# Optimization experiments

Hardware: AMD Instinct MI355X
Metric: run time of the kernel (lower is better)

The kernel has to match this reference:

```python
import jax, jax.numpy as jnp
import numpy as np

NUM_TIMESCALES = 16
MAX_TIME = 100.0
N_HEADS = 4
MLP_WIDTH = 128
HIDDEN_EACH = 128  # hidden_size // attn_n_heads = 512 // 4


def setup_inputs() -> dict:
    key = jax.random.key(0)
    ks = jax.random.split(key, 8)
    B, ROWS_PER_PAT, V = 32, 64, 32
    R = B * ROWS_PER_PAT
    # patient i has counts[i] observations, laid out row-major in its block of rows
    counts = 512 + 16 * np.arange(B)
    M = np.zeros((R, V), np.int32)
    for i in range(B):
        flat = M[i * ROWS_PER_PAT:(i + 1) * ROWS_PER_PAT].reshape(-1)
        flat[:counts[i]] = 1
    n_obs = int(counts.sum())        # 24320
    max_n_obs = int(counts.max())    # 1008
    n_in = 2 * NUM_TIMESCALES + 2    # 34

    def lin(k, o, i_):
        kw, kb = jax.random.split(k)
        return (jax.random.normal(kw, (o, i_)) * (1.0 / np.sqrt(i_)),
                jax.random.normal(kb, (o,)) * 0.01)

    W0, b0 = lin(ks[0], MLP_WIDTH, n_in)
    W1, b1 = lin(ks[1], MLP_WIDTH, MLP_WIDTH)
    W2, b2 = lin(ks[2], HIDDEN_EACH, MLP_WIDTH)
    Wq, bq = lin(ks[3], HIDDEN_EACH, HIDDEN_EACH)
    Wk, bk = lin(ks[4], HIDDEN_EACH, HIDDEN_EACH)
    return {
        "times": jax.random.uniform(ks[5], (R,)) * MAX_TIME,
        "time_ptr": jnp.arange(R + 1),
        "X": jax.random.normal(ks[6], (R, V)),
        "M": jnp.asarray(M),
        "obs_idx": jnp.repeat(jnp.arange(B), ROWS_PER_PAT),
        "pat_idx": jnp.arange(B),
        "W0": W0, "b0": b0, "W1": W1, "b1": b1, "W2": W2, "b2": b2,
        "Wq": Wq, "bq": bq, "Wk": Wk, "bk": bk,
        "n_obs": n_obs, "max_n_obs": max_n_obs,
    }


def reference(times, time_ptr, X, M, obs_idx, pat_idx,
              W0, b0, W1, b1, W2, b2, Wq, bq, Wk, bk, n_obs, max_n_obs):
    B = pat_idx.shape[0]
    # --- ragged scatter: (time_row, var) observations -> padded per-patient sets ---
    rows, cols = jnp.nonzero(M, size=n_obs)          # row-major, grouped by patient
    p = obs_idx[rows]                                # patient id per observation
    vals = X[rows, cols]
    t_arr = jnp.repeat(times, jnp.diff(time_ptr), total_repeat_length=X.shape[0])
    t = t_arr[rows]
    lens = jnp.bincount(p, length=B)
    starts = jnp.cumsum(lens) - lens
    pos = jnp.arange(n_obs) - starts[p]              # within-patient slot index
    Sv = jnp.zeros((B, max_n_obs), X.dtype).at[p, pos].set(cols.astype(X.dtype))
    Sx = jnp.zeros((B, max_n_obs), X.dtype).at[p, pos].set(vals)
    St = jnp.zeros((B, max_n_obs), X.dtype).at[p, pos].set(t)
    pad = jnp.arange(max_n_obs)[None, :] >= lens[:, None]   # True = padding
    # --- time embedding + feature concat: [sin, cos, var, value] ---
    timescales = MAX_TIME ** jnp.linspace(0.0, 1.0, NUM_TIMESCALES)
    st = St[..., None] / timescales
    new_X = jnp.concatenate([jnp.sin(st), jnp.cos(st), Sv[..., None], Sx[..., None]], axis=-1)
    # --- encoder MLP (depth 3 -> 1 hidden layer, eval mode: dropout is identity) ---
    h = jax.nn.relu(new_X @ W0.T + b0)
    h = jax.nn.relu(h @ W1.T + b1)
    enc = h @ W2.T + b2                              # [B, L, 128]
    # --- masked self-attention weights (only q/k matter; output is discarded) ---
    L = max_n_obs
    hd = HIDDEN_EACH // N_HEADS
    q = (enc @ Wq.T + bq).reshape(B, L, N_HEADS, hd)
    k = (enc @ Wk.T + bk).reshape(B, L, N_HEADS, hd)
    scores = jnp.einsum('blhd,bmhd->bhlm', q, k) / np.sqrt(hd)
    scores = jnp.where(pad[:, None, None, :], -1e30, scores)
    attn = jax.nn.softmax(scores, axis=-1)           # [B, H, L, L]
    w = attn[:, :, -1, :]                            # last-query attention row
    summed = jnp.einsum('bhl,ble->bhe', w, enc)      # [B, H, 128]
    return summed.reshape(B, -1)                     # [B, 512]
```

## Files before the change

### kernel.cpp

```cpp
#include <hip/hip_runtime.h>

#define B_PAT 32
#define RTOT 2048
#define NV 32
#define LMAX 1008
#define NTS 16
#define NIN 64
#define TLD 72
#define HW 128
#define LDSP 136
#define NCH 16
#define CH 63
#define ELD 132
#define RLD 136

typedef __attribute__((ext_vector_type(8))) short short8;
typedef __attribute__((ext_vector_type(4))) float floatx4;

__device__ __forceinline__ ushort f2b(float f) {
  unsigned int x = __float_as_uint(f);
  unsigned int r = (x + 0x7FFFu + ((x >> 16) & 1u)) >> 16;
  return (ushort)r;
}
__device__ __forceinline__ unsigned int pack2(ushort lo, ushort hi) {
  return (unsigned int)lo | ((unsigned int)hi << 16);
}
__device__ __forceinline__ float tscale(int i) {
  return exp2f((float)i * (6.643856189774724f / 15.0f));
}

__global__ __launch_bounds__(256) void kP(
    const float* __restrict__ times, const int* __restrict__ time_ptr,
    const float* __restrict__ X, const int* __restrict__ M,
    const int* __restrict__ obs_idx,
    const float* __restrict__ W0, const float* __restrict__ b0,
    const float* __restrict__ W1, const float* __restrict__ b1,
    const float* __restrict__ W2, const float* __restrict__ b2,
    const float* __restrict__ Wq, const float* __restrict__ bq,
    const float* __restrict__ Wk,
    int* __restrict__ pbase_g, int* __restrict__ rowstart_g,
    int* __restrict__ lens, float* __restrict__ trow_g,
    ushort* __restrict__ W0p, ushort* __restrict__ W1b, ushort* __restrict__ W2b,
    float* __restrict__ r_all)
{
  const int b = blockIdx.x;
  const int t = threadIdx.x;
  if (b >= B_PAT) {
    if (b == B_PAT) {
      for (int i = t; i < HW * NIN; i += 256) {
        int n = i >> 6, k = i & 63;
        W0p[i] = (k < 34) ? f2b(W0[n * 34 + k]) : (ushort)0;
      }
    } else if (b == B_PAT + 1) {
      for (int i = t; i < HW * HW; i += 256) W1b[i] = f2b(W1[i]);
    } else {
      for (int i = t; i < HW * HW; i += 256) W2b[i] = f2b(W2[i]);
    }
    return;
  }
  __shared__ int rs_s, re_s;
  __shared__ int cnt_s[64];
  __shared__ int pbase_s[65];
  __shared__ float tval_s[64];
  __shared__ int qrc[3];
  __shared__ float x_s[64];
  __shared__ float h0[HW], h1[HW], eq[HW], q_s[HW], part[256];
  for (int r = t * 8; r < t * 8 + 8; ++r) {
    if (obs_idx[r] == b) {
      if (r == 0 || obs_idx[r - 1] != b) rs_s = r;
      if (r == RTOT - 1 || obs_idx[r + 1] != b) re_s = r + 1;
    }
  }
  __syncthreads();
  const int rs = rs_s, re = re_s;
  const int n = re - rs;
  if (t < 64) {
    int c = 0;
    if (t < n) {
      const int4* mp = (const int4*)(M + (size_t)(rs + t) * NV);
#pragma unroll
      for (int q = 0; q < 8; ++q) {
        int4 m4 = mp[q];
        c += (m4.x != 0) + (m4.y != 0) + (m4.z != 0) + (m4.w != 0);
      }
      int lo = 0, hi = RTOT - 1, r = rs + t;
      while (lo < hi) { int mid = (lo + hi + 1) >> 1; if (time_ptr[mid] <= r) lo = mid; else hi = mid - 1; }
      tval_s[t] = times[lo];
      trow_g[r] = times[lo];
    }
    cnt_s[t] = c;
  }
  __syncthreads();
  if (t < 64) {
    int incl = cnt_s[t];
    for (int off = 1; off < 64; off <<= 1) {
      int v = __shfl_up(incl, off);
      if (t >= off) incl += v;
    }
    pbase_s[t + 1] = incl;
    if (t == 0) pbase_s[0] = 0;
  }
  __syncthreads();
  const int len = pbase_s[64];
  if (t < 65) pbase_g[b * 65 + t] = pbase_s[t];
  if (t == 0) { rowstart_g[b] = rs; lens[b] = len; }
  if (t == 0) {
    if (LMAX - 1 < len) {
      int lr = 0;
      while (pbase_s[lr + 1] <= LMAX - 1) ++lr;
      int k = (LMAX - 1) - pbase_s[lr], col = 0;
      for (int cc = 0; cc < NV; ++cc)
        if (M[(size_t)(rs + lr) * NV + cc] != 0) { if (k == 0) { col = cc; break; } --k; }
      qrc[0] = lr; qrc[1] = col; qrc[2] = 1;
    } else qrc[2] = 0;
  }
  if (t < 64) x_s[t] = 0.0f;
  __syncthreads();
  if (qrc[2] == 0) {
    if (t >= 16 && t < 32) x_s[t] = 1.0f;
  } else {
    int lr = qrc[0], col = qrc[1];
    if (t < 16) {
      float a = tval_s[lr] / tscale(t);
      x_s[t] = sinf(a); x_s[16 + t] = cosf(a);
    }
    if (t == 0) { x_s[32] = (float)col; x_s[33] = X[(size_t)(rs + lr) * NV + col]; }
  }
  __syncthreads();
  if (t < HW) {
    float a = b0[t];
#pragma unroll 2
    for (int k = 0; k < 34; ++k) a += W0[t * 34 + k] * x_s[k];
    h0[t] = fmaxf(a, 0.0f);
  }
  __syncthreads();
  {
    int oo = t & 127, hf = t >> 7;
    float a = 0.f;
    const float* wr = W1 + oo * HW + hf * 64;
#pragma unroll 8
    for (int k = 0; k < 64; ++k) a += wr[k] * h0[hf * 64 + k];
    part[t] = a;
  }
  __syncthreads();
  if (t < HW) h1[t] = fmaxf(part[t] + part[t + 128] + b1[t], 0.0f);
  __syncthreads();
  {
    int oo = t & 127, hf = t >> 7;
    float a = 0.f;
    const float* wr = W2 + oo * HW + hf * 64;
#pragma unroll 8
    for (int k = 0; k < 64; ++k) a += wr[k] * h1[hf * 64 + k];
    part[t] = a;
  }
  __syncthreads();
  if (t < HW) eq[t] = part[t] + part[t + 128] + b2[t];
  __syncthreads();
  {
    int oo = t & 127, hf = t >> 7;
    float a = 0.f;
    const float* wr = Wq + oo * HW + hf * 64;
#pragma unroll 8
    for (int k = 0; k < 64; ++k) a += wr[k] * eq[hf * 64 + k];
    part[t] = a;
  }
  __syncthreads();
  if (t < HW) q_s[t] = part[t] + part[t + 128] + bq[t];
  __syncthreads();
  const float scale = 0.17677669529663687f;
  for (int idx = t; idx < 512; idx += 256) {
    int h = idx >> 7, e = idx & 127;
    float a = 0.f;
#pragma unroll 8
    for (int d = 0; d < 32; ++d) a += Wk[(h * 32 + d) * HW + e] * q_s[h * 32 + d];
    r_all[b * 512 + idx] = a * scale;
  }
}

__global__ __launch_bounds__(512) void kF(
    const int* __restrict__ M, const float* __restrict__ X,
    const int* __restrict__ pbase_g, const int* __restrict__ rowstart_g,
    const int* __restrict__ lens, const float* __restrict__ trow_g,
    const ushort* __restrict__ W0p, const float* __restrict__ b0,
    const ushort* __restrict__ W1b, const float* __restrict__ b1,
    const ushort* __restrict__ W2b, const float* __restrict__ b2,
    const float* __restrict__ r_all, float* __restrict__ partial,
    float2* __restrict__ mxsm)
{
  const int bx = blockIdx.x;
  const int b = bx >> 4, c = bx & 15;
  const int t = threadIdx.x;
  const int len = lens[b];
  const int start = c * CH;
  int valid = len - start; if (valid > CH) valid = CH;
  if (valid <= 0) {
    if (t < 4) mxsm[bx * 4 + t] = make_float2(-1e30f, 0.0f);
    return;
  }
  __shared__ ushort tile[64 * TLD];
  __shared__ ushort bufA[64 * LDSP];
  __shared__ ushort bufB[64 * LDSP];
  __shared__ float encs[64 * ELD];
  __shared__ float r_s[4 * RLD];
  __shared__ float lg[4 * 64];
  __shared__ unsigned int umask[64];
  __shared__ float tval[64];
  __shared__ int pbase_s[65];
  __shared__ float inv_ts[NTS];
  __shared__ float mx_s[4], sm_s[4];
  const int rs = rowstart_g[b];
  {
    uint4 z = make_uint4(0u, 0u, 0u, 0u);
    uint4* tp = (uint4*)tile;
    for (int i = t; i < 64 * TLD / 8; i += 512) tp[i] = z;
    if (t < 512) r_s[(t >> 7) * RLD + (t & 127)] = r_all[b * 512 + t];
  }
  if (t < 64) {
    const int4* mp = (const int4*)(M + (size_t)(rs + t) * NV);
    unsigned int mk = 0;
#pragma unroll
    for (int q8 = 0; q8 < 8; ++q8) {
      int4 m4 = mp[q8];
      mk |= (m4.x != 0 ? 1u : 0u) << (q8 * 4);
      mk |= (m4.y != 0 ? 1u : 0u) << (q8 * 4 + 1);
      mk |= (m4.z != 0 ? 1u : 0u) << (q8 * 4 + 2);
      mk |= (m4.w != 0 ? 1u : 0u) << (q8 * 4 + 3);
    }
    umask[t] = mk;
    tval[t] = trow_g[rs + t];
  } else if (t < 129) {
    pbase_s[t - 64] = pbase_g[b * 65 + (t - 64)];
  } else if (t >= 136 && t < 136 + NTS) {
    inv_ts[t - 136] = 1.0f / tscale(t - 136);
  }
  __syncthreads();
  {
    int pos = t >> 3, sub = t & 7;
    if (pos < valid && sub < 5) {
      int gpos = start + pos;
      int lo = 0, hi = 63;
      while (lo < hi) { int mid = (lo + hi + 1) >> 1; if (pbase_s[mid] <= gpos) lo = mid; else hi = mid - 1; }
      int lrow = lo;
      int rank = gpos - pbase_s[lrow];
      unsigned int m = umask[lrow];
      for (int i = 0; i < rank; ++i) m &= m - 1;
      int col = (m != 0u) ? __builtin_ctz(m) : 0;
      float tv = tval[lrow];
      unsigned int* dst = (unsigned int*)(tile + pos * TLD);
      if (sub < 2) {
#pragma unroll
        for (int w = 0; w < 4; ++w) {
          int i0 = sub * 8 + 2 * w;
          dst[sub * 4 + w] = pack2(f2b(__sinf(tv * inv_ts[i0])), f2b(__sinf(tv * inv_ts[i0 + 1])));
        }
      } else if (sub < 4) {
#pragma unroll
        for (int w = 0; w < 4; ++w) {
          int i0 = (sub - 2) * 8 + 2 * w;
          dst[8 + (sub - 2) * 4 + w] = pack2(f2b(__cosf(tv * inv_ts[i0])), f2b(__cosf(tv * inv_ts[i0 + 1])));
        }
      } else {
        dst[16] = pack2(f2b((float)col), f2b(X[(size_t)(rs + lrow) * NV + col]));
      }
    }
  }
  __syncthreads();
  const int wv = t >> 6, lane = t & 63;
  const int m16 = lane & 15, quad = lane >> 4;
  const int rg = wv & 3, nh = wv >> 2;
  const int rowl = rg * 16 + m16;
  {
    const short8* ar = (const short8*)(tile + rowl * TLD);
    short8 a0 = ar[quad];
    short8 a1 = ar[4 + quad];
#pragma unroll
    for (int nt = 0; nt < 4; ++nt) {
      int nn = nh * 64 + nt * 16 + m16;
      const short8* br = (const short8*)(W0p + nn * NIN);
      floatx4 acc = {0.f, 0.f, 0.f, 0.f};
      acc = __builtin_amdgcn_mfma_f32_16x16x32_bf16(a0, br[quad], acc, 0, 0, 0);
      acc = __builtin_amdgcn_mfma_f32_16x16x32_bf16(a1, br[4 + quad], acc, 0, 0, 0);
      float bias = b0[nn];
#pragma unroll
      for (int i = 0; i < 4; ++i) {
        float vv = fmaxf(acc[i] + bias, 0.0f);
        bufA[(rg * 16 + quad * 4 + i) * LDSP + nn] = f2b(vv);
      }
    }
  }
  __syncthreads();
  {
#pragma unroll
    for (int nt = 0; nt < 4; ++nt) {
      int nn = nh * 64 + nt * 16 + m16;
      floatx4 acc = {0.f, 0.f, 0.f, 0.f};
#pragma unroll
      for (int ks = 0; ks < 4; ++ks) {
        short8 a = *(const short8*)(bufA + rowl * LDSP + ks * 32 + quad * 8);
        short8 bb = *(const short8*)(W1b + nn * HW + ks * 32 + quad * 8);
        acc = __builtin_amdgcn_mfma_f32_16x16x32_bf16(a, bb, acc, 0, 0, 0);
      }
      float bias = b1[nn];
#pragma unroll
      for (int i = 0; i < 4; ++i) {
        float vv = fmaxf(acc[i] + bias, 0.0f);
        bufB[(rg * 16 + quad * 4 + i) * LDSP + nn] = f2b(vv);
      }
    }
  }
  __syncthreads();
  {
#pragma unroll
    for (int nt = 0; nt < 4; ++nt) {
      int nn = nh * 64 + nt * 16 + m16;
      floatx4 acc = {0.f, 0.f, 0.f, 0.f};
#pragma unroll
      for (int ks = 0; ks < 4; ++ks) {
        short8 a = *(const short8*)(bufB + rowl * LDSP + ks * 32 + quad * 8);
        short8 bb = *(const short8*)(W2b + nn * HW + ks * 32 + quad * 8);
        acc = __builtin_amdgcn_mfma_f32_16x16x32_bf16(a, bb, acc, 0, 0, 0);
      }
      float bias = b2[nn];
#pragma unroll
      for (int i = 0; i < 4; ++i)
        encs[(rg * 16 + quad * 4 + i) * ELD + nn] = acc[i] + bias;
    }
  }
  __syncthreads();
  {
    int m = t >> 3, h = t & 7;
    if (m < valid && h < 4) {
      const float4* ev = (const float4*)(&encs[m * ELD]);
      const float4* rv = (const float4*)(&r_s[h * RLD]);
      float acc = 0.f;
#pragma unroll
      for (int e4 = 0; e4 < 32; ++e4) {
        float4 v = ev[e4], r = rv[e4];
        acc += v.x * r.x + v.y * r.y + v.z * r.z + v.w * r.w;
      }
      lg[h * 64 + m] = acc;
    }
  }
  __syncthreads();
  if (wv < 4) {
    float v = (lane < valid) ? lg[wv * 64 + lane] : -1e30f;
    float mx = v;
#pragma unroll
    for (int o = 32; o >= 1; o >>= 1) mx = fmaxf(mx, __shfl_xor(mx, o));
    float p = (lane < valid) ? __expf(v - mx) : 0.f;
    lg[wv * 64 + lane] = p;
    float sm = p;
#pragma unroll
    for (int o = 32; o >= 1; o >>= 1) sm += __shfl_xor(sm, o);
    if (lane == 0) { mx_s[wv] = mx; sm_s[wv] = sm; }
  }
  __syncthreads();
  {
    int h = t >> 7, e = t & 127;
    float acc = 0.f;
    for (int m = 0; m < valid; ++m)
      acc += lg[h * 64 + m] * encs[m * ELD + e];
    partial[(size_t)bx * 512 + t] = acc;
  }
  if (t < 4) mxsm[bx * 4 + t] = make_float2(mx_s[t], sm_s[t]);
}

__global__ __launch_bounds__(256) void kK(
    const float* __restrict__ partial, const float2* __restrict__ mxsm,
    float* __restrict__ out)
{
  const int b = blockIdx.x;
  const int tid = threadIdx.x;
  __shared__ float f_s[NCH * 4];
  if (tid < 4) {
    int h = tid;
    float2 v[NCH];
    float M = -1e30f;
#pragma unroll
    for (int c = 0; c < NCH; ++c) {
      v[c] = mxsm[(b * NCH + c) * 4 + h];
      if (v[c].y > 0.f) M = fmaxf(M, v[c].x);
    }
    float S = 0.f;
#pragma unroll
    for (int c = 0; c < NCH; ++c)
      if (v[c].y > 0.f) S += v[c].y * expf(v[c].x - M);
    float invS = 1.0f / S;
#pragma unroll
    for (int c = 0; c < NCH; ++c)
      f_s[c * 4 + h] = (v[c].y > 0.f) ? expf(v[c].x - M) * invS : 0.f;
  }
  __syncthreads();
  for (int idx = tid; idx < 512; idx += 256) {
    int h = idx >> 7;
    float acc = 0.f;
#pragma unroll
    for (int c = 0; c < NCH; ++c) {
      float f = f_s[c * 4 + h];
      if (f > 0.f) acc += partial[((size_t)(b * NCH + c)) * 512 + idx] * f;
    }
    out[b * 512 + idx] = acc;
  }
}

extern "C" void kernel_launch(void* const* d_in, const int* in_sizes, int n_in,
                              void* d_out, int out_size, void* d_ws, size_t ws_size,
                              hipStream_t stream) {
  const float* times = (const float*)d_in[0];
  const int* time_ptr = (const int*)d_in[1];
  const float* X = (const float*)d_in[2];
  const int* M = (const int*)d_in[3];
  const int* obs_idx = (const int*)d_in[4];
  const float* W0 = (const float*)d_in[6];
  const float* b0 = (const float*)d_in[7];
  const float* W1 = (const float*)d_in[8];
  const float* b1 = (const float*)d_in[9];
  const float* W2 = (const float*)d_in[10];
  const float* b2 = (const float*)d_in[11];
  const float* Wq = (const float*)d_in[12];
  const float* bq = (const float*)d_in[13];
  const float* Wk = (const float*)d_in[14];
  float* out = (float*)d_out;

  char* ws = (char*)d_ws;
  size_t off = 0;
  int* pbase_g = (int*)(ws + off); off += (size_t)B_PAT * 65 * 4;
  int* rowstart_g = (int*)(ws + off); off += 256;
  int* lens = (int*)(ws + off); off += 256;
  float* trow_g = (float*)(ws + off); off += RTOT * 4;
  ushort* W0p = (ushort*)(ws + off); off += (size_t)HW * NIN * 2;
  ushort* W1b = (ushort*)(ws + off); off += (size_t)HW * HW * 2;
  ushort* W2b = (ushort*)(ws + off); off += (size_t)HW * HW * 2;
  float* r_all = (float*)(ws + off); off += (size_t)B_PAT * 512 * 4;
  float* partial = (float*)(ws + off); off += (size_t)B_PAT * NCH * 512 * 4;
  float2* mxsm = (float2*)(ws + off); off += (size_t)B_PAT * NCH * 4 * 8;

  kP<<<B_PAT + 3, 256, 0, stream>>>(times, time_ptr, X, M, obs_idx,
                                    W0, b0, W1, b1, W2, b2, Wq, bq, Wk,
                                    pbase_g, rowstart_g, lens, trow_g,
                                    W0p, W1b, W2b, r_all);
  kF<<<B_PAT * NCH, 512, 0, stream>>>(M, X, pbase_g, rowstart_g, lens, trow_g,
                                      W0p, b0, W1b, b1, W2b, b2, r_all,
                                      partial, mxsm);
  kK<<<B_PAT, 256, 0, stream>>>(partial, mxsm, out);
}
```

Measured before the change: 141.0 us.

## Fuse final softmax-combine kernel into kF via last-block atomic counter

```diff
diff --git a/kernel.cpp b/kernel.cpp
--- a/kernel.cpp
+++ b/kernel.cpp
@@ -41,7 +41,7 @@
     int* __restrict__ pbase_g, int* __restrict__ rowstart_g,
     int* __restrict__ lens, float* __restrict__ trow_g,
     ushort* __restrict__ W0p, ushort* __restrict__ W1b, ushort* __restrict__ W2b,
-    float* __restrict__ r_all)
+    float* __restrict__ r_all, int* __restrict__ cnt_g)
 {
   const int b = blockIdx.x;
   const int t = threadIdx.x;
@@ -58,6 +58,7 @@
     }
     return;
   }
+  if (t == 0) cnt_g[b] = 0;
   __shared__ int rs_s, re_s;
   __shared__ int cnt_s[64];
   __shared__ int pbase_s[65];
@@ -185,7 +186,8 @@
     const ushort* __restrict__ W1b, const float* __restrict__ b1,
     const ushort* __restrict__ W2b, const float* __restrict__ b2,
     const float* __restrict__ r_all, float* __restrict__ partial,
-    float2* __restrict__ mxsm)
+    float2* __restrict__ mxsm, int* __restrict__ cnt_g,
+    float* __restrict__ out)
 {
   const int bx = blockIdx.x;
   const int b = bx >> 4, c = bx & 15;
@@ -193,10 +195,6 @@
   const int len = lens[b];
   const int start = c * CH;
   int valid = len - start; if (valid > CH) valid = CH;
-  if (valid <= 0) {
-    if (t < 4) mxsm[bx * 4 + t] = make_float2(-1e30f, 0.0f);
-    return;
-  }
   __shared__ ushort tile[64 * TLD];
   __shared__ ushort bufA[64 * LDSP];
   __shared__ ushort bufB[64 * LDSP];
@@ -208,198 +206,204 @@
   __shared__ int pbase_s[65];
   __shared__ float inv_ts[NTS];
   __shared__ float mx_s[4], sm_s[4];
-  const int rs = rowstart_g[b];
-  {
-    uint4 z = make_uint4(0u, 0u, 0u, 0u);
-    uint4* tp = (uint4*)tile;
-    for (int i = t; i < 64 * TLD / 8; i += 512) tp[i] = z;
-    if (t < 512) r_s[(t >> 7) * RLD + (t & 127)] = r_all[b * 512 + t];
-  }
-  if (t < 64) {
-    const int4* mp = (const int4*)(M + (size_t)(rs + t) * NV);
-    unsigned int mk = 0;
-#pragma unroll
-    for (int q8 = 0; q8 < 8; ++q8) {
-      int4 m4 = mp[q8];
-      mk |= (m4.x != 0 ? 1u : 0u) << (q8 * 4);
-      mk |= (m4.y != 0 ? 1u : 0u) << (q8 * 4 + 1);
-      mk |= (m4.z != 0 ? 1u : 0u) << (q8 * 4 + 2);
-      mk |= (m4.w != 0 ? 1u : 0u) << (q8 * 4 + 3);
-    }
-    umask[t] = mk;
-    tval[t] = trow_g[rs + t];
-  } else if (t < 129) {
-    pbase_s[t - 64] = pbase_g[b * 65 + (t - 64)];
-  } else if (t >= 136 && t < 136 + NTS) {
-    inv_ts[t - 136] = 1.0f / tscale(t - 136);
-  }
-  __syncthreads();
-  {
-    int pos = t >> 3, sub = t & 7;
-    if (pos < valid && sub < 5) {
-      int gpos = start + pos;
-      int lo = 0, hi = 63;
-      while (lo < hi) { int mid = (lo + hi + 1) >> 1; if (pbase_s[mid] <= gpos) lo = mid; else hi = mid - 1; }
-      int lrow = lo;
-      int rank = gpos - pbase_s[lrow];
-      unsigned int m = umask[lrow];
-      for (int i = 0; i < rank; ++i) m &= m - 1;
-      int col = (m != 0u) ? __builtin_ctz(m) : 0;
-      float tv = tval[lrow];
-      unsigned int* dst = (unsigned int*)(tile + pos * TLD);
-      if (sub < 2) {
-#pragma unroll
-        for (int w = 0; w < 4; ++w) {
-          int i0 = sub * 8 + 2 * w;
-          dst[sub * 4 + w] = pack2(f2b(__sinf(tv * inv_ts[i0])), f2b(__sinf(tv * inv_ts[i0 + 1])));
-        }
-      } else if (sub < 4) {
-#pragma unroll
-        for (int w = 0; w < 4; ++w) {
-          int i0 = (sub - 2) * 8 + 2 * w;
-          dst[8 + (sub - 2) * 4 + w] = pack2(f2b(__cosf(tv * inv_ts[i0])), f2b(__cosf(tv * inv_ts[i0 + 1])));
-        }
-      } else {
-        dst[16] = pack2(f2b((float)col), f2b(X[(size_t)(rs + lrow) * NV + col]));
-      }
-    }
-  }
-  __syncthreads();
-  const int wv = t >> 6, lane = t & 63;
-  const int m16 = lane & 15, quad = lane >> 4;
-  const int rg = wv & 3, nh = wv >> 2;
-  const int rowl = rg * 16 + m16;
-  {
-    const short8* ar = (const short8*)(tile + rowl * TLD);
-    short8 a0 = ar[quad];
-    short8 a1 = ar[4 + quad];
-#pragma unroll
-    for (int nt = 0; nt < 4; ++nt) {
-      int nn = nh * 64 + nt * 16 + m16;
-      const short8* br = (const short8*)(W0p + nn * NIN);
-      floatx4 acc = {0.f, 0.f, 0.f, 0.f};
-      acc = __builtin_amdgcn_mfma_f32_16x16x32_bf16(a0, br[quad], acc, 0, 0, 0);
-      acc = __builtin_amdgcn_mfma_f32_16x16x32_bf16(a1, br[4 + quad], acc, 0, 0, 0);
-      float bias = b0[nn];
-#pragma unroll
-      for (int i = 0; i < 4; ++i) {
-        float vv = fmaxf(acc[i] + bias, 0.0f);
-        bufA[(rg * 16 + quad * 4 + i) * LDSP + nn] = f2b(vv);
-      }
-    }
-  }
-  __syncthreads();
-  {
-#pragma unroll
-    for (int nt = 0; nt < 4; ++nt) {
-      int nn = nh * 64 + nt * 16 + m16;
-      floatx4 acc = {0.f, 0.f, 0.f, 0.f};
-#pragma unroll
-      for (int ks = 0; ks < 4; ++ks) {
-        short8 a = *(const short8*)(bufA + rowl * LDSP + ks * 32 + quad * 8);
-        short8 bb = *(const short8*)(W1b + nn * HW + ks * 32 + quad * 8);
-        acc = __builtin_amdgcn_mfma_f32_16x16x32_bf16(a, bb, acc, 0, 0, 0);
-      }
-      float bias = b1[nn];
-#pragma unroll
-      for (int i = 0; i < 4; ++i) {
-        float vv = fmaxf(acc[i] + bias, 0.0f);
-        bufB[(rg * 16 + quad * 4 + i) * LDSP + nn] = f2b(vv);
-      }
-    }
-  }
-  __syncthreads();
-  {
-#pragma unroll
-    for (int nt = 0; nt < 4; ++nt) {
-      int nn = nh * 64 + nt * 16 + m16;
-      floatx4 acc = {0.f, 0.f, 0.f, 0.f};
-#pragma unroll
-      for (int ks = 0; ks < 4; ++ks) {
-        short8 a = *(const short8*)(bufB + rowl * LDSP + ks * 32 + quad * 8);
-        short8 bb = *(const short8*)(W2b + nn * HW + ks * 32 + quad * 8);
-        acc = __builtin_amdgcn_mfma_f32_16x16x32_bf16(a, bb, acc, 0, 0, 0);
-      }
-      float bias = b2[nn];
-#pragma unroll
-      for (int i = 0; i < 4; ++i)
-        encs[(rg * 16 + quad * 4 + i) * ELD + nn] = acc[i] + bias;
-    }
-  }
-  __syncthreads();
-  {
-    int m = t >> 3, h = t & 7;
-    if (m < valid && h < 4) {
-      const float4* ev = (const float4*)(&encs[m * ELD]);
-      const float4* rv = (const float4*)(&r_s[h * RLD]);
+  __shared__ int last_s;
+  __shared__ float f_s[NCH * 4];
+  if (valid > 0) {
+    const int rs = rowstart_g[b];
+    r_s[(t >> 7) * RLD + (t & 127)] = r_all[b * 512 + t];
+    if (t < 64) {
+      const int4* mp = (const int4*)(M + (size_t)(rs + t) * NV);
+      unsigned int mk = 0;
+#pragma unroll
+      for (int q8 = 0; q8 < 8; ++q8) {
+        int4 m4 = mp[q8];
+        mk |= (m4.x != 0 ? 1u : 0u) << (q8 * 4);
+        mk |= (m4.y != 0 ? 1u : 0u) << (q8 * 4 + 1);
+        mk |= (m4.z != 0 ? 1u : 0u) << (q8 * 4 + 2);
+        mk |= (m4.w != 0 ? 1u : 0u) << (q8 * 4 + 3);
+      }
+      umask[t] = mk;
+      tval[t] = trow_g[rs + t];
+    } else if (t < 129) {
+      pbase_s[t - 64] = pbase_g[b * 65 + (t - 64)];
+    } else if (t >= 136 && t < 136 + NTS) {
+      inv_ts[t - 136] = 1.0f / tscale(t - 136);
+    }
+    __syncthreads();
+    {
+      int pos = t >> 3, sub = t & 7;
+      if (pos < valid) {
+        unsigned int* dst = (unsigned int*)(tile + pos * TLD);
+        if (sub < 5) {
+          int gpos = start + pos;
+          int lo = 0, hi = 63;
+          while (lo < hi) { int mid = (lo + hi + 1) >> 1; if (pbase_s[mid] <= gpos) lo = mid; else hi = mid - 1; }
+          int lrow = lo;
+          int rank = gpos - pbase_s[lrow];
+          unsigned int m = umask[lrow];
+          for (int i = 0; i < rank; ++i) m &= m - 1;
+          int col = (m != 0u) ? __builtin_ctz(m) : 0;
+          float tv = tval[lrow];
+          if (sub < 2) {
+#pragma unroll
+            for (int w = 0; w < 4; ++w) {
+              int i0 = sub * 8 + 2 * w;
+              dst[sub * 4 + w] = pack2(f2b(__sinf(tv * inv_ts[i0])), f2b(__sinf(tv * inv_ts[i0 + 1])));
+            }
+          } else if (sub < 4) {
+#pragma unroll
+            for (int w = 0; w < 4; ++w) {
+              int i0 = (sub - 2) * 8 + 2 * w;
+              dst[8 + (sub - 2) * 4 + w] = pack2(f2b(__cosf(tv * inv_ts[i0])), f2b(__cosf(tv * inv_ts[i0 + 1])));
+            }
+          } else {
+            dst[16] = pack2(f2b((float)col), f2b(X[(size_t)(rs + lrow) * NV + col]));
+          }
+        } else {
+          int d0 = 17 + (sub - 5) * 5;
+#pragma unroll
+          for (int w = 0; w < 5; ++w) dst[d0 + w] = 0u;
+        }
+      }
+    }
+    __syncthreads();
+    const int wv = t >> 6, lane = t & 63;
+    const int m16 = lane & 15, quad = lane >> 4;
+    const int rg = wv & 3, nh = wv >> 2;
+    const int rowl = rg * 16 + m16;
+    {
+      const short8* ar = (const short8*)(tile + rowl * TLD);
+      short8 a0 = ar[quad];
+      short8 a1 = ar[4 + quad];
+#pragma unroll
+      for (int nt = 0; nt < 4; ++nt) {
+        int nn = nh * 64 + nt * 16 + m16;
+        const short8* br = (const short8*)(W0p + nn * NIN);
+        floatx4 acc = {0.f, 0.f, 0.f, 0.f};
+        acc = __builtin_amdgcn_mfma_f32_16x16x32_bf16(a0, br[quad], acc, 0, 0, 0);
+        acc = __builtin_amdgcn_mfma_f32_16x16x32_bf16(a1, br[4 + quad], acc, 0, 0, 0);
+        float bias = b0[nn];
+#pragma unroll
+        for (int i = 0; i < 4; ++i) {
+          float vv = fmaxf(acc[i] + bias, 0.0f);
+          bufA[(rg * 16 + quad * 4 + i) * LDSP + nn] = f2b(vv);
+        }
+      }
+    }
+    __syncthreads();
+    {
+#pragma unroll
+      for (int nt = 0; nt < 4; ++nt) {
+        int nn = nh * 64 + nt * 16 + m16;
+        floatx4 acc = {0.f, 0.f, 0.f, 0.f};
+#pragma unroll
+        for (int ks = 0; ks < 4; ++ks) {
+          short8 a = *(const short8*)(bufA + rowl * LDSP + ks * 32 + quad * 8);
+          short8 bb = *(const short8*)(W1b + nn * HW + ks * 32 + quad * 8);
+          acc = __builtin_amdgcn_mfma_f32_16x16x32_bf16(a, bb, acc, 0, 0, 0);
+        }
+        float bias = b1[nn];
+#pragma unroll
+        for (int i = 0; i < 4; ++i) {
+          float vv = fmaxf(acc[i] + bias, 0.0f);
+          bufB[(rg * 16 + quad * 4 + i) * LDSP + nn] = f2b(vv);
+        }
+      }
+    }
+    __syncthreads();
+    {
+#pragma unroll
+      for (int nt = 0; nt < 4; ++nt) {
+        int nn = nh * 64 + nt * 16 + m16;
+        floatx4 acc = {0.f, 0.f, 0.f, 0.f};
+#pragma unroll
+        for (int ks = 0; ks < 4; ++ks) {
+          short8 a = *(const short8*)(bufB + rowl * LDSP + ks * 32 + quad * 8);
+          short8 bb = *(const short8*)(W2b + nn * HW + ks * 32 + quad * 8);
+          acc = __builtin_amdgcn_mfma_f32_16x16x32_bf16(a, bb, acc, 0, 0, 0);
+        }
+        float bias = b2[nn];
+#pragma unroll
+        for (int i = 0; i < 4; ++i)
+          encs[(rg * 16 + quad * 4 + i) * ELD + nn] = acc[i] + bias;
+      }
+    }
+    __syncthreads();
+    {
+      int m = t >> 3, h = t & 7;
+      if (m < valid && h < 4) {
+        const float4* ev = (const float4*)(&encs[m * ELD]);
+        const float4* rv = (const float4*)(&r_s[h * RLD]);
+        float acc = 0.f;
+#pragma unroll
+        for (int e4 = 0; e4 < 32; ++e4) {
+          float4 v = ev[e4], r = rv[e4];
+          acc += v.x * r.x + v.y * r.y + v.z * r.z + v.w * r.w;
+        }
+        lg[h * 64 + m] = acc;
+      }
+    }
+    __syncthreads();
+    if (wv < 4) {
+      float v = (lane < valid) ? lg[wv * 64 + lane] : -1e30f;
+      float mx = v;
+#pragma unroll
+      for (int o = 32; o >= 1; o >>= 1) mx = fmaxf(mx, __shfl_xor(mx, o));
+      float p = (lane < valid) ? __expf(v - mx) : 0.f;
+      lg[wv * 64 + lane] = p;
+      float sm = p;
+#pragma unroll
+      for (int o = 32; o >= 1; o >>= 1) sm += __shfl_xor(sm, o);
+      if (lane == 0) { mx_s[wv] = mx; sm_s[wv] = sm; }
+    }
+    __syncthreads();
+    {
+      int h = t >> 7;
       float acc = 0.f;
-#pragma unroll
-      for (int e4 = 0; e4 < 32; ++e4) {
-        float4 v = ev[e4], r = rv[e4];
-        acc += v.x * r.x + v.y * r.y + v.z * r.z + v.w * r.w;
-      }
-      lg[h * 64 + m] = acc;
-    }
-  }
-  __syncthreads();
-  if (wv < 4) {
-    float v = (lane < valid) ? lg[wv * 64 + lane] : -1e30f;
-    float mx = v;
-#pragma unroll
-    for (int o = 32; o >= 1; o >>= 1) mx = fmaxf(mx, __shfl_xor(mx, o));
-    float p = (lane < valid) ? __expf(v - mx) : 0.f;
-    lg[wv * 64 + lane] = p;
-    float sm = p;
-#pragma unroll
-    for (int o = 32; o >= 1; o >>= 1) sm += __shfl_xor(sm, o);
-    if (lane == 0) { mx_s[wv] = mx; sm_s[wv] = sm; }
-  }
-  __syncthreads();
-  {
-    int h = t >> 7, e = t & 127;
-    float acc = 0.f;
-    for (int m = 0; m < valid; ++m)
-      acc += lg[h * 64 + m] * encs[m * ELD + e];
-    partial[(size_t)bx * 512 + t] = acc;
-  }
-  if (t < 4) mxsm[bx * 4 + t] = make_float2(mx_s[t], sm_s[t]);
-}
-
-__global__ __launch_bounds__(256) void kK(
-    const float* __restrict__ partial, const float2* __restrict__ mxsm,
-    float* __restrict__ out)
-{
-  const int b = blockIdx.x;
-  const int tid = threadIdx.x;
-  __shared__ float f_s[NCH * 4];
-  if (tid < 4) {
-    int h = tid;
-    float2 v[NCH];
-    float M = -1e30f;
-#pragma unroll
-    for (int c = 0; c < NCH; ++c) {
-      v[c] = mxsm[(b * NCH + c) * 4 + h];
-      if (v[c].y > 0.f) M = fmaxf(M, v[c].x);
-    }
-    float S = 0.f;
-#pragma unroll
-    for (int c = 0; c < NCH; ++c)
-      if (v[c].y > 0.f) S += v[c].y * expf(v[c].x - M);
-    float invS = 1.0f / S;
-#pragma unroll
-    for (int c = 0; c < NCH; ++c)
-      f_s[c * 4 + h] = (v[c].y > 0.f) ? expf(v[c].x - M) * invS : 0.f;
-  }
-  __syncthreads();
-  for (int idx = tid; idx < 512; idx += 256) {
-    int h = idx >> 7;
-    float acc = 0.f;
-#pragma unroll
-    for (int c = 0; c < NCH; ++c) {
-      float f = f_s[c * 4 + h];
-      if (f > 0.f) acc += partial[((size_t)(b * NCH + c)) * 512 + idx] * f;
-    }
-    out[b * 512 + idx] = acc;
+      int e = t & 127;
+      for (int m = 0; m < valid; ++m)
+        acc += lg[h * 64 + m] * encs[m * ELD + e];
+      partial[(size_t)bx * 512 + t] = acc;
+    }
+    if (t < 4) mxsm[bx * 4 + t] = make_float2(mx_s[t], sm_s[t]);
+  } else {
+    if (t < 4) mxsm[bx * 4 + t] = make_float2(-1e30f, 0.0f);
+  }
+  __syncthreads();
+  __threadfence();
+  if (t == 0) last_s = (atomicAdd(&cnt_g[b], 1) == NCH - 1) ? 1 : 0;
+  __syncthreads();
+  if (last_s) {
+    __threadfence();
+    if (t < 4) {
+      int h = t;
+      float2 v[NCH];
+      float Mx = -1e30f;
+#pragma unroll
+      for (int cc = 0; cc < NCH; ++cc) {
+        v[cc] = mxsm[(b * NCH + cc) * 4 + h];
+        if (v[cc].y > 0.f) Mx = fmaxf(Mx, v[cc].x);
+      }
+      float S = 0.f;
+#pragma unroll
+      for (int cc = 0; cc < NCH; ++cc)
+        if (v[cc].y > 0.f) S += v[cc].y * __expf(v[cc].x - Mx);
+      float invS = 1.0f / S;
+#pragma unroll
+      for (int cc = 0; cc < NCH; ++cc)
+        f_s[cc * 4 + h] = (v[cc].y > 0.f) ? __expf(v[cc].x - Mx) * invS : 0.f;
+    }
+    __syncthreads();
+    {
+      int h = t >> 7;
+      float acc = 0.f;
+#pragma unroll
+      for (int cc = 0; cc < NCH; ++cc) {
+        float f = f_s[cc * 4 + h];
+        if (f > 0.f) acc += partial[((size_t)(b * NCH + cc)) * 512 + t] * f;
+      }
+      out[b * 512 + t] = acc;
+    }
   }
 }
 
@@ -427,6 +431,7 @@
   int* pbase_g = (int*)(ws + off); off += (size_t)B_PAT * 65 * 4;
   int* rowstart_g = (int*)(ws + off); off += 256;
   int* lens = (int*)(ws + off); off += 256;
+  int* cnt_g = (int*)(ws + off); off += 256;
   float* trow_g = (float*)(ws + off); off += RTOT * 4;
   ushort* W0p = (ushort*)(ws + off); off += (size_t)HW * NIN * 2;
   ushort* W1b = (ushort*)(ws + off); off += (size_t)HW * HW * 2;
@@ -438,9 +443,8 @@
   kP<<<B_PAT + 3, 256, 0, stream>>>(times, time_ptr, X, M, obs_idx,
                                     W0, b0, W1, b1, W2, b2, Wq, bq, Wk,
                                     pbase_g, rowstart_g, lens, trow_g,
-                                    W0p, W1b, W2b, r_all);
+                                    W0p, W1b, W2b, r_all, cnt_g);
   kF<<<B_PAT * NCH, 512, 0, stream>>>(M, X, pbase_g, rowstart_g, lens, trow_g,
                                       W0p, b0, W1b, b1, W2b, b2, r_all,
-                                      partial, mxsm);
-  kK<<<B_PAT, 256, 0, stream>>>(partial, mxsm, out);
-}
+                                      partial, mxsm, cnt_g, out);
+}
```

After: 215.8 us. 1.53x slower.
